# Optimization experiments

Hardware: AMD Instinct MI355X
Metric: run time of the kernel (lower is better)

Reference implementation:

```python
import jax, jax.numpy as jnp
import numpy as np


def _normalize(x, axis=-1, eps=1e-12):
    n = jnp.linalg.norm(x, axis=axis, keepdims=True)
    return x / jnp.maximum(n, eps)


def _mlp(x, w1, b1, w2, b2):
    return jnp.maximum(x @ w1 + b1, 0.0) @ w2 + b2


def _quat_mul(a, b):
    # openfold (w, x, y, z) convention, Hamilton product
    aw, ax, ay, az = a[..., 0], a[..., 1], a[..., 2], a[..., 3]
    bw, bx, by, bz = b[..., 0], b[..., 1], b[..., 2], b[..., 3]
    return jnp.stack([
        aw * bw - ax * bx - ay * by - az * bz,
        aw * bx + ax * bw + ay * bz - az * by,
        aw * by - ax * bz + ay * bw + az * bx,
        aw * bz + ax * by - ay * bx + az * bw], axis=-1)


def _quat_rotate(q, v):
    # rotate vector v by unit quaternion q
    w = q[..., :1]
    u = q[..., 1:]
    t = 2.0 * jnp.cross(u, v)
    return v + w * t + jnp.cross(u, t)


def _conj(q):
    return q * jnp.asarray([1.0, -1.0, -1.0, -1.0], dtype=q.dtype)


def setup_inputs() -> dict:
    B, N, P, H, E, M = 2, 384, 128, 64, 32, 64
    key = jax.random.key(0)
    ks = iter(jax.random.split(key, 64))

    def nrm(shape):
        return jax.random.normal(next(ks), shape, dtype=jnp.float32)

    inp = {
        "frames_q": _normalize(nrm((B, N, 4))),
        "frames_x": nrm((B, N, 3)),
        "torsions": nrm((B, N, 7, 2)),
        "h": nrm((B, N, H)),
        "e": nrm((B, N, N, E)),
        "node_mask": jnp.ones((B, N), dtype=bool),
        "pocket_h": nrm((B, P, H)),
        "pocket_e": nrm((B, N, P, E)),
        "pocket_q": _normalize(nrm((B, P, 4))),
        "pocket_x": nrm((B, P, 3)),
        "pocket_mask": jnp.ones((B, P), dtype=bool),
    }
    # 2-layer MLPs with transition_size = 64
    for name, (fin, fout) in {"msg": (2 * H + E + 9, M), "feat": (H + M, H),
                              "tr": (M, 3), "qu": (M, 4), "to": (M, 14)}.items():
        inp[f"{name}_w1"] = nrm((fin, 64)) / np.sqrt(fin)
        inp[f"{name}_b1"] = nrm((64,)) * 0.01
        inp[f"{name}_w2"] = nrm((64, fout)) / np.sqrt(64)
        inp[f"{name}_b2"] = nrm((fout,)) * 0.01
    return inp


def reference(frames_q, frames_x, torsions, h, e, node_mask, pocket_h, pocket_e,
              pocket_q, pocket_x, pocket_mask,
              msg_w1, msg_b1, msg_w2, msg_b2,
              feat_w1, feat_b1, feat_w2, feat_b2,
              tr_w1, tr_b1, tr_w2, tr_b2,
              qu_w1, qu_b1, qu_w2, qu_b2,
              to_w1, to_b1, to_w2, to_b2):
    B, N, Hd = h.shape
    P = pocket_h.shape[-2]

    q_all = jnp.concatenate([frames_q, pocket_q], axis=-2)  # [B, N+P, 4]
    x_all = jnp.concatenate([frames_x, pocket_x], axis=-2)  # [B, N+P, 3]

    eye = jnp.eye(N, dtype=bool)
    mm = jnp.concatenate([
        node_mask[:, :, None] & node_mask[:, None, :] & ~eye,
        node_mask[:, :, None] & pocket_mask[:, None, :]], axis=-1)  # [B, N, N+P]

    vec = frames_x[:, :, None, :] - x_all[:, None, :, :]  # [B, N, N+P, 3]
    d2 = jnp.sum(vec * vec, axis=-1)                       # [B, N, N+P]
    qdot = jnp.abs(jnp.sum(frames_q[:, :, None, :] * q_all[:, None, :, :], axis=-1))

    # global -> local frame of node j applied to node i: R_j^T (x_i - t_j)
    qc = _conj(q_all)[:, None, :, :]                       # [B, 1, N+P, 4]
    local_x = _quat_rotate(qc, vec)                        # [B, N, N+P, 3]
    local_q = _quat_mul(qc, jnp.broadcast_to(frames_q[:, :, None, :], (B, N, N + P, 4)))

    feat = jnp.concatenate([
        jnp.broadcast_to(h[:, :, None, :], (B, N, N + P, Hd)),
        jnp.broadcast_to(jnp.concatenate([h, pocket_h], axis=-2)[:, None, :, :], (B, N, N + P, Hd)),
        jnp.concatenate([e, pocket_e], axis=-2),
        local_x, local_q, d2[..., None], qdot[..., None]], axis=-1)

    m = _mlp(feat, msg_w1, msg_b1, msg_w2, msg_b2) * mm[..., None]  # [B, N, N+P, M]
    msum = jnp.sum(m, axis=-2)                                      # [B, N, M]

    o = _mlp(jnp.concatenate([h, msum], axis=-1), feat_w1, feat_b1, feat_w2, feat_b2)

    dx = _mlp(m, tr_w1, tr_b1, tr_w2, tr_b2) * mm[..., None]        # [B, N, N+P, 3]

    ident = jnp.asarray([1.0, 0.0, 0.0, 0.0], dtype=frames_q.dtype)
    dq = _mlp(msum, qu_w1, qu_b1, qu_w2, qu_b2)
    dq = _normalize(jnp.where(node_mask[..., None], dq, ident))
    upd_q = _quat_mul(frames_q, dq)
    upd_q = _normalize(jnp.where(node_mask[..., None], upd_q, ident))

    qn_all = _normalize(q_all)
    gdx = jnp.sum(_quat_rotate(qn_all[:, None, :, :], dx), axis=-2)  # [B, N, 3]
    n_nb = (node_mask.sum(-1) + pocket_mask.sum(-1) - 1).astype(frames_x.dtype)
    upd_x = frames_x + gdx / n_nb[:, None, None]

    upd_torsions = _normalize(_mlp(msum, to_w1, to_b1, to_w2, to_b2).reshape(torsions.shape))

    return upd_q, upd_x, upd_torsions, o
```

## Files before the change

### kernel.cpp

```cpp
#include <hip/hip_runtime.h>
#include <math.h>

#define BB 2
#define NN 384
#define PP 128
#define HH 64
#define EE 32
#define NP 512
#define K1S 136
#define K2S 72

#define X_OFF (BB*NN*4)
#define T_OFF (X_OFF + BB*NN*3)
#define O_OFF (T_OFF + BB*NN*14)

using bf16x8 = __attribute__((ext_vector_type(8))) __bf16;
using f32x4  = __attribute__((ext_vector_type(4))) float;

__device__ __forceinline__ f32x4 MFMA(bf16x8 a, bf16x8 b, f32x4 c) {
  return __builtin_amdgcn_mfma_f32_16x16x32_bf16(a, b, c, 0, 0, 0);
}
__device__ __forceinline__ bf16x8 LDF(const __bf16* base, int off) {
  return *(const bf16x8*)(base + off);
}
__device__ __forceinline__ bf16x8 pack8(f32x4 lo, f32x4 hi) {
  bf16x8 r;
  r[0]=(__bf16)lo[0]; r[1]=(__bf16)lo[1]; r[2]=(__bf16)lo[2]; r[3]=(__bf16)lo[3];
  r[4]=(__bf16)hi[0]; r[5]=(__bf16)hi[1]; r[6]=(__bf16)hi[2]; r[7]=(__bf16)hi[3];
  return r;
}
__device__ __forceinline__ bf16x8 pack8v(float4 lo, float4 hi) {
  bf16x8 r;
  r[0]=(__bf16)lo.x; r[1]=(__bf16)lo.y; r[2]=(__bf16)lo.z; r[3]=(__bf16)lo.w;
  r[4]=(__bf16)hi.x; r[5]=(__bf16)hi.y; r[6]=(__bf16)hi.z; r[7]=(__bf16)hi.w;
  return r;
}
__device__ __forceinline__ int rowpos(int n) {
  const int t = (n>>5)*2 + ((n>>2)&1);
  const int q = ((n>>3)&3)*4 + (n&3);
  return t*16 + q;
}

__global__ __launch_bounds__(512, 2) void egnn_edge_swapped(
    const float* __restrict__ frames_q, const float* __restrict__ frames_x,
    const float* __restrict__ h, const float* __restrict__ e,
    const int* __restrict__ node_mask,
    const float* __restrict__ pocket_h, const float* __restrict__ pe,
    const float* __restrict__ pocket_q, const float* __restrict__ pocket_x,
    const int* __restrict__ pocket_mask,
    const float* __restrict__ w1, const float* __restrict__ b1,
    const float* __restrict__ w2, const float* __restrict__ b2,
    const float* __restrict__ tw1, const float* __restrict__ tb1,
    const float* __restrict__ tw2, const float* __restrict__ tb2,
    float* __restrict__ msum_ws, float* __restrict__ gdx_ws)
{
  __shared__ __align__(16) __bf16 s_w1p[64*K1S];
  __shared__ __align__(16) __bf16 s_w2p[64*K2S];
  __shared__ __align__(16) __bf16 s_tw1p[64*K2S];
  __shared__ __align__(16) __bf16 s_tw2p[16*K2S];
  __shared__ __align__(16) __bf16 s_geo[NP*16 + 8];
  __shared__ __align__(16) float s_qn[NP*4];
  __shared__ float s_maskf[NP];
  __shared__ float s_b2[64], s_tb1[64], s_tb2[4];
  __shared__ float s_msum[64], s_gdx[3];

  const int tid = threadIdx.x;
  const int b = blockIdx.x / NN, i = blockIdx.x % NN;

  for (int idx = tid; idx < 64*128; idx += 512) {
    const int n = idx & 63, k = idx >> 6;
    float v = 0.f;
    if      (k < 64)  v = w1[(64 + k)*64 + n];
    else if (k < 96)  v = w1[(128 + (k-64))*64 + n];
    else if (k < 105) v = w1[(160 + (k-96))*64 + n];
    if (k != 105) s_w1p[rowpos(n)*K1S + k] = (__bf16)v;
  }
  for (int idx = tid; idx < 64*64; idx += 512) {
    const int n = idx & 63, k = idx >> 6;
    s_w2p[rowpos(n)*K2S + k]  = (__bf16)w2[k*64 + n];
    s_tw1p[rowpos(n)*K2S + k] = (__bf16)tw1[k*64 + n];
  }
  for (int idx = tid; idx < 16*64; idx += 512) {
    const int row = idx >> 6, k = idx & 63;
    s_tw2p[row*K2S + k] = (__bf16)((row < 3) ? tw2[k*3 + row] : 0.f);
  }
  if (tid < 64) { s_b2[tid] = b2[tid]; s_tb1[tid] = tb1[tid]; s_msum[tid] = 0.f; }
  if (tid < 8)  s_geo[NP*16 + tid] = (__bf16)0.f;
  if (tid < 3)  { s_tb2[tid] = tb2[tid]; s_gdx[tid] = 0.f; }

  {
    const int n = tid >> 3, part = tid & 7;
    const float* hi = &h[(b*NN + i)*HH];
    float a = 0.f;
#pragma unroll
    for (int c = 0; c < 8; ++c) a = fmaf(hi[part*8 + c], w1[(part*8 + c)*64 + n], a);
    a += __shfl_xor(a, 1); a += __shfl_xor(a, 2); a += __shfl_xor(a, 4);
    if (part == 0) s_w1p[rowpos(n)*K1S + 105] = (__bf16)(a + b1[n]);
  }

  {
    const int j = tid;
    const int maski = node_mask[b*NN + i];
    const float qi0 = frames_q[(b*NN+i)*4+0], qi1 = frames_q[(b*NN+i)*4+1],
                qi2 = frames_q[(b*NN+i)*4+2], qi3 = frames_q[(b*NN+i)*4+3];
    const float xi0 = frames_x[(b*NN+i)*3+0], xi1 = frames_x[(b*NN+i)*3+1],
                xi2 = frames_x[(b*NN+i)*3+2];
    float qj0,qj1,qj2,qj3, xj0,xj1,xj2; int mj;
    if (j < NN) {
      const float4 q4 = *(const float4*)&frames_q[(b*NN+j)*4];
      qj0=q4.x; qj1=q4.y; qj2=q4.z; qj3=q4.w;
      xj0=frames_x[(b*NN+j)*3+0]; xj1=frames_x[(b*NN+j)*3+1]; xj2=frames_x[(b*NN+j)*3+2];
      mj = (node_mask[b*NN+j] != 0) && (j != i);
    } else {
      const int jp = j - NN;
      const float4 q4 = *(const float4*)&pocket_q[(b*PP+jp)*4];
      qj0=q4.x; qj1=q4.y; qj2=q4.z; qj3=q4.w;
      xj0=pocket_x[(b*PP+jp)*3+0]; xj1=pocket_x[(b*PP+jp)*3+1]; xj2=pocket_x[(b*PP+jp)*3+2];
      mj = (pocket_mask[b*PP+jp] != 0);
    }
    const float v0 = xi0 - xj0, v1 = xi1 - xj1, v2 = xi2 - xj2;
    const float d2 = v0*v0 + v1*v1 + v2*v2;
    const float qdot = fabsf(qi0*qj0 + qi1*qj1 + qi2*qj2 + qi3*qj3);
    const float cw = qj0, cx = -qj1, cy = -qj2, cz = -qj3;
    const float t0 = 2.f*(cy*v2 - cz*v1);
    const float t1 = 2.f*(cz*v0 - cx*v2);
    const float t2 = 2.f*(cx*v1 - cy*v0);
    const float lx0 = v0 + cw*t0 + (cy*t2 - cz*t1);
    const float lx1 = v1 + cw*t1 + (cz*t0 - cx*t2);
    const float lx2 = v2 + cw*t2 + (cx*t1 - cy*t0);
    const float lq0 = cw*qi0 - cx*qi1 - cy*qi2 - cz*qi3;
    const float lq1 = cw*qi1 + cx*qi0 + cy*qi3 - cz*qi2;
    const float lq2 = cw*qi2 - cx*qi3 + cy*qi0 + cz*qi1;
    const float lq3 = cw*qi3 + cx*qi2 - cy*qi1 + cz*qi0;
    __bf16* g = &s_geo[j*16];
    g[0]=(__bf16)lx0; g[1]=(__bf16)lx1; g[2]=(__bf16)lx2; g[3]=(__bf16)lq0;
    g[4]=(__bf16)lq1; g[5]=(__bf16)lq2; g[6]=(__bf16)lq3; g[7]=(__bf16)d2;
    g[8]=(__bf16)qdot; g[9]=(__bf16)1.f;
    g[10]=(__bf16)0.f; g[11]=(__bf16)0.f; g[12]=(__bf16)0.f;
    g[13]=(__bf16)0.f; g[14]=(__bf16)0.f; g[15]=(__bf16)0.f;
    s_maskf[j] = (maski && mj) ? 1.f : 0.f;
    const float inv = 1.f / fmaxf(sqrtf(qj0*qj0 + qj1*qj1 + qj2*qj2 + qj3*qj3), 1e-12f);
    float4* qn = (float4*)&s_qn[j*4];
    *qn = make_float4(qj0*inv, qj1*inv, qj2*inv, qj3*inv);
  }
  __syncthreads();

  const int wv = tid >> 6, lane = tid & 63;
  const int l15 = lane & 15, lg = lane >> 4;

  bf16x8 tw2f[2];
  tw2f[0] = *(const bf16x8*)&s_tw2p[l15*K2S +  0 + lg*8];
  tw2f[1] = *(const bf16x8*)&s_tw2p[l15*K2S + 32 + lg*8];

  float b2r[16], tb1r[16];
#pragma unroll
  for (int t2 = 0; t2 < 4; ++t2)
#pragma unroll
    for (int r = 0; r < 4; ++r) {
      const int n2 = (t2>>1)*32 + lg*8 + (t2&1)*4 + r;
      b2r[t2*4 + r]  = s_b2[n2];
      tb1r[t2*4 + r] = s_tb1[n2];
    }
  const float tb2r0 = s_tb2[0], tb2r1 = s_tb2[1], tb2r2 = s_tb2[2];

  float msacc[16];
#pragma unroll
  for (int v = 0; v < 16; ++v) msacc[v] = 0.f;
  float gx0 = 0.f, gx1 = 0.f, gx2 = 0.f;

  const int o1base = l15*K1S + lg*8;
  const int o2base = l15*K2S + lg*8;

#define LOADSTRIP(S, H0_,H1_,H2_,H3_,E0_,E1_) do {                          \
    const int jbase_ = wv*64 + (S)*16;                                      \
    const int j_ = jbase_ + l15;                                            \
    const float *hj_, *ej_;                                                 \
    if (jbase_ < NN) {                                                      \
      hj_ = &h[(b*NN + j_)*HH];                                             \
      ej_ = &e[((b*NN + i)*NN + j_)*EE];                                    \
    } else {                                                                \
      const int jp_ = j_ - NN;                                              \
      hj_ = &pocket_h[(b*PP + jp_)*HH];                                     \
      ej_ = &pe[((b*NN + i)*PP + jp_)*EE];                                  \
    }                                                                       \
    H0_ = *(const float4*)&hj_[lg*8];                                       \
    H1_ = *(const float4*)&hj_[lg*8 + 4];                                   \
    H2_ = *(const float4*)&hj_[32 + lg*8];                                  \
    H3_ = *(const float4*)&hj_[32 + lg*8 + 4];                              \
    E0_ = *(const float4*)&ej_[lg*8];                                       \
    E1_ = *(const float4*)&ej_[lg*8 + 4];                                   \
  } while (0)

  float4 cH0, cH1, cH2, cH3, cE0, cE1;
  float4 nH0, nH1, nH2, nH3, nE0, nE1;
  LOADSTRIP(0, cH0, cH1, cH2, cH3, cE0, cE1);

#pragma unroll
  for (int s = 0; s < 4; ++s) {
    if (s < 3) LOADSTRIP(s+1, nH0, nH1, nH2, nH3, nE0, nE1);

    int o1 = o1base; asm volatile("" : "+v"(o1));
    int o2 = o2base; asm volatile("" : "+v"(o2));

    const int j = wv*64 + s*16 + l15;
    const float mask_f = s_maskf[j];

    const bf16x8 bf0 = pack8v(cH0, cH1);
    const bf16x8 bf1 = pack8v(cH2, cH3);
    const bf16x8 bf2 = pack8v(cE0, cE1);
    const bf16x8 bf3 = *(const bf16x8*)&s_geo[(lg < 2) ? (j*16 + lg*8) : NP*16];

    const f32x4 zero4 = {0.f, 0.f, 0.f, 0.f};
    f32x4 a0 = MFMA(LDF(s_w1p, o1 + 0*16*K1S +  0), bf0, zero4);
    a0 = MFMA(LDF(s_w1p, o1 + 0*16*K1S + 32), bf1, a0);
    a0 = MFMA(LDF(s_w1p, o1 + 0*16*K1S + 64), bf2, a0);
    a0 = MFMA(LDF(s_w1p, o1 + 0*16*K1S + 96), bf3, a0);
    f32x4 a1 = MFMA(LDF(s_w1p, o1 + 1*16*K1S +  0), bf0, zero4);
    a1 = MFMA(LDF(s_w1p, o1 + 1*16*K1S + 32), bf1, a1);
    a1 = MFMA(LDF(s_w1p, o1 + 1*16*K1S + 64), bf2, a1);
    a1 = MFMA(LDF(s_w1p, o1 + 1*16*K1S + 96), bf3, a1);
#pragma unroll
    for (int r = 0; r < 4; ++r) { a0[r] = fmaxf(a0[r], 0.f); a1[r] = fmaxf(a1[r], 0.f); }
    const bf16x8 hb0 = pack8(a0, a1);
    f32x4 a2 = MFMA(LDF(s_w1p, o1 + 2*16*K1S +  0), bf0, zero4);
    a2 = MFMA(LDF(s_w1p, o1 + 2*16*K1S + 32), bf1, a2);
    a2 = MFMA(LDF(s_w1p, o1 + 2*16*K1S + 64), bf2, a2);
    a2 = MFMA(LDF(s_w1p, o1 + 2*16*K1S + 96), bf3, a2);
    f32x4 a3 = MFMA(LDF(s_w1p, o1 + 3*16*K1S +  0), bf0, zero4);
    a3 = MFMA(LDF(s_w1p, o1 + 3*16*K1S + 32), bf1, a3);
    a3 = MFMA(LDF(s_w1p, o1 + 3*16*K1S + 64), bf2, a3);
    a3 = MFMA(LDF(s_w1p, o1 + 3*16*K1S + 96), bf3, a3);
#pragma unroll
    for (int r = 0; r < 4; ++r) { a2[r] = fmaxf(a2[r], 0.f); a3[r] = fmaxf(a3[r], 0.f); }
    const bf16x8 hb1 = pack8(a2, a3);

    f32x4 c0 = MFMA(LDF(s_w2p, o2 + 0*16*K2S +  0), hb0, zero4);
    c0 = MFMA(LDF(s_w2p, o2 + 0*16*K2S + 32), hb1, c0);
    f32x4 c1 = MFMA(LDF(s_w2p, o2 + 1*16*K2S +  0), hb0, zero4);
    c1 = MFMA(LDF(s_w2p, o2 + 1*16*K2S + 32), hb1, c1);
#pragma unroll
    for (int r = 0; r < 4; ++r) {
      c0[r] = (c0[r] + b2r[0*4+r]) * mask_f;  msacc[0*4+r] += c0[r];
      c1[r] = (c1[r] + b2r[1*4+r]) * mask_f;  msacc[1*4+r] += c1[r];
    }
    const bf16x8 mb0 = pack8(c0, c1);
    f32x4 c2 = MFMA(LDF(s_w2p, o2 + 2*16*K2S +  0), hb0, zero4);
    c2 = MFMA(LDF(s_w2p, o2 + 2*16*K2S + 32), hb1, c2);
    f32x4 c3 = MFMA(LDF(s_w2p, o2 + 3*16*K2S +  0), hb0, zero4);
    c3 = MFMA(LDF(s_w2p, o2 + 3*16*K2S + 32), hb1, c3);
#pragma unroll
    for (int r = 0; r < 4; ++r) {
      c2[r] = (c2[r] + b2r[2*4+r]) * mask_f;  msacc[2*4+r] += c2[r];
      c3[r] = (c3[r] + b2r[3*4+r]) * mask_f;  msacc[3*4+r] += c3[r];
    }
    const bf16x8 mb1 = pack8(c2, c3);

    f32x4 d0 = MFMA(LDF(s_tw1p, o2 + 0*16*K2S +  0), mb0, zero4);
    d0 = MFMA(LDF(s_tw1p, o2 + 0*16*K2S + 32), mb1, d0);
    f32x4 d1 = MFMA(LDF(s_tw1p, o2 + 1*16*K2S +  0), mb0, zero4);
    d1 = MFMA(LDF(s_tw1p, o2 + 1*16*K2S + 32), mb1, d1);
#pragma unroll
    for (int r = 0; r < 4; ++r) {
      d0[r] = fmaxf(d0[r] + tb1r[0*4+r], 0.f);
      d1[r] = fmaxf(d1[r] + tb1r[1*4+r], 0.f);
    }
    const bf16x8 thb0 = pack8(d0, d1);
    f32x4 d2f = MFMA(LDF(s_tw1p, o2 + 2*16*K2S +  0), mb0, zero4);
    d2f = MFMA(LDF(s_tw1p, o2 + 2*16*K2S + 32), mb1, d2f);
    f32x4 d3 = MFMA(LDF(s_tw1p, o2 + 3*16*K2S +  0), mb0, zero4);
    d3 = MFMA(LDF(s_tw1p, o2 + 3*16*K2S + 32), mb1, d3);
#pragma unroll
    for (int r = 0; r < 4; ++r) {
      d2f[r] = fmaxf(d2f[r] + tb1r[2*4+r], 0.f);
      d3[r]  = fmaxf(d3[r]  + tb1r[3*4+r], 0.f);
    }
    const bf16x8 thb1 = pack8(d2f, d3);

    f32x4 dacc = MFMA(tw2f[0], thb0, zero4);
    dacc = MFMA(tw2f[1], thb1, dacc);

    if (lg == 0) {
      const float dx0 = (dacc[0] + tb2r0) * mask_f;
      const float dx1 = (dacc[1] + tb2r1) * mask_f;
      const float dx2 = (dacc[2] + tb2r2) * mask_f;
      const float4 qn = *(const float4*)&s_qn[j*4];
      const float w = qn.x, ux = qn.y, uy = qn.z, uz = qn.w;
      const float r0 = 2.f*(uy*dx2 - uz*dx1);
      const float r1 = 2.f*(uz*dx0 - ux*dx2);
      const float r2 = 2.f*(ux*dx1 - uy*dx0);
      gx0 += dx0 + w*r0 + (uy*r2 - uz*r1);
      gx1 += dx1 + w*r1 + (uz*r0 - ux*r2);
      gx2 += dx2 + w*r2 + (ux*r1 - uy*r0);
    }

    if (s < 3) {
      cH0 = nH0; cH1 = nH1; cH2 = nH2; cH3 = nH3; cE0 = nE0; cE1 = nE1;
    }
  }
#undef LOADSTRIP

#pragma unroll
  for (int v = 0; v < 16; ++v) {
    float x = msacc[v];
    x += __shfl_xor(x, 1); x += __shfl_xor(x, 2);
    x += __shfl_xor(x, 4); x += __shfl_xor(x, 8);
    if (l15 == 0) {
      const int n2 = (v>>3)*32 + lg*8 + ((v>>2)&1)*4 + (v&3);
      atomicAdd(&s_msum[n2], x);
    }
  }
  {
    float v0 = (lg == 0) ? gx0 : 0.f;
    float v1 = (lg == 0) ? gx1 : 0.f;
    float v2 = (lg == 0) ? gx2 : 0.f;
#pragma unroll
    for (int sft = 1; sft < 64; sft <<= 1) {
      v0 += __shfl_xor(v0, sft); v1 += __shfl_xor(v1, sft); v2 += __shfl_xor(v2, sft);
    }
    if (lane == 0) { atomicAdd(&s_gdx[0], v0); atomicAdd(&s_gdx[1], v1); atomicAdd(&s_gdx[2], v2); }
  }
  __syncthreads();
  if (tid < 64) msum_ws[(b*NN + i)*64 + tid] = s_msum[tid];
  if (tid >= 64 && tid < 67) gdx_ws[(b*NN + i)*3 + (tid - 64)] = s_gdx[tid - 64];
}

__global__ __launch_bounds__(64) void egnn_node_kernel(
    const float* __restrict__ frames_q, const float* __restrict__ frames_x,
    const float* __restrict__ h,
    const int* __restrict__ node_mask, const int* __restrict__ pocket_mask,
    const float* __restrict__ fw1, const float* __restrict__ fb1,
    const float* __restrict__ fw2, const float* __restrict__ fb2,
    const float* __restrict__ qw1, const float* __restrict__ qb1,
    const float* __restrict__ qw2, const float* __restrict__ qb2,
    const float* __restrict__ tow1, const float* __restrict__ tob1,
    const float* __restrict__ tow2, const float* __restrict__ tob2,
    const float* __restrict__ msum_ws, const float* __restrict__ gdx_ws,
    float* __restrict__ out)
{
  const int t  = threadIdx.x;
  const int bi = blockIdx.x;
  const int b = bi / NN, i = bi % NN;
  __shared__ float s_h[64], s_ms[64], s_hid[64], s_tmp[16];

  s_h[t]  = h[(b*NN+i)*HH + t];
  s_ms[t] = msum_ws[(b*NN+i)*64 + t];

  int cnt = 0;
  for (int k = t; k < NN; k += 64) cnt += (node_mask[b*NN+k] != 0);
  for (int k = t; k < PP; k += 64) cnt += (pocket_mask[b*PP+k] != 0);
  cnt += __shfl_xor(cnt,1); cnt += __shfl_xor(cnt,2); cnt += __shfl_xor(cnt,4);
  cnt += __shfl_xor(cnt,8); cnt += __shfl_xor(cnt,16); cnt += __shfl_xor(cnt,32);
  const float n_nb = (float)(cnt - 1);

  __syncthreads();
  float a = fb1[t];
  for (int k = 0; k < 64; ++k) a = fmaf(s_h[k],  fw1[k*64 + t], a);
  for (int k = 0; k < 64; ++k) a = fmaf(s_ms[k], fw1[(64+k)*64 + t], a);
  s_hid[t] = fmaxf(a, 0.f);
  __syncthreads();
  float ov = fb2[t];
  for (int k = 0; k < 64; ++k) ov = fmaf(s_hid[k], fw2[k*64 + t], ov);
  out[O_OFF + (b*NN+i)*64 + t] = ov;

  __syncthreads();
  float aq = qb1[t];
  for (int k = 0; k < 64; ++k) aq = fmaf(s_ms[k], qw1[k*64 + t], aq);
  s_hid[t] = fmaxf(aq, 0.f);
  __syncthreads();
  if (t < 4) {
    float d = qb2[t];
    for (int k = 0; k < 64; ++k) d = fmaf(s_hid[k], qw2[k*4 + t], d);
    s_tmp[t] = d;
  }
  __syncthreads();
  if (t == 0) {
    const int mi = node_mask[b*NN+i];
    float d0,d1,d2,d3;
    if (mi) { d0=s_tmp[0]; d1=s_tmp[1]; d2=s_tmp[2]; d3=s_tmp[3]; }
    else    { d0=1.f; d1=0.f; d2=0.f; d3=0.f; }
    float nrm = fmaxf(sqrtf(d0*d0+d1*d1+d2*d2+d3*d3), 1e-12f);
    d0/=nrm; d1/=nrm; d2/=nrm; d3/=nrm;
    const float q0=frames_q[(b*NN+i)*4+0], q1=frames_q[(b*NN+i)*4+1],
                q2=frames_q[(b*NN+i)*4+2], q3=frames_q[(b*NN+i)*4+3];
    float u0 = q0*d0 - q1*d1 - q2*d2 - q3*d3;
    float u1 = q0*d1 + q1*d0 + q2*d3 - q3*d2;
    float u2 = q0*d2 - q1*d3 + q2*d0 + q3*d1;
    float u3 = q0*d3 + q1*d2 - q2*d1 + q3*d0;
    if (!mi) { u0=1.f; u1=0.f; u2=0.f; u3=0.f; }
    float nrm2 = fmaxf(sqrtf(u0*u0+u1*u1+u2*u2+u3*u3), 1e-12f);
    out[(b*NN+i)*4+0]=u0/nrm2; out[(b*NN+i)*4+1]=u1/nrm2;
    out[(b*NN+i)*4+2]=u2/nrm2; out[(b*NN+i)*4+3]=u3/nrm2;
  }
  if (t < 3) {
    out[X_OFF + (b*NN+i)*3 + t] = frames_x[(b*NN+i)*3+t] + gdx_ws[(b*NN+i)*3+t] / n_nb;
  }

  __syncthreads();
  float at = tob1[t];
  for (int k = 0; k < 64; ++k) at = fmaf(s_ms[k], tow1[k*64 + t], at);
  s_hid[t] = fmaxf(at, 0.f);
  __syncthreads();
  if (t < 14) {
    float v = tob2[t];
    for (int k = 0; k < 64; ++k) v = fmaf(s_hid[k], tow2[k*14 + t], v);
    s_tmp[t] = v;
  }
  __syncthreads();
  if (t < 14) {
    const int p = t & ~1;
    const float a0 = s_tmp[p], a1 = s_tmp[p+1];
    const float nrm = fmaxf(sqrtf(a0*a0 + a1*a1), 1e-12f);
    out[T_OFF + (b*NN+i)*14 + t] = s_tmp[t] / nrm;
  }
}

extern "C" void kernel_launch(void* const* d_in, const int* in_sizes, int n_in,
                              void* d_out, int out_size, void* d_ws, size_t ws_size,
                              hipStream_t stream) {
  const float* frames_q    = (const float*)d_in[0];
  const float* frames_x    = (const float*)d_in[1];
  const float* h           = (const float*)d_in[3];
  const float* e           = (const float*)d_in[4];
  const int*   node_mask   = (const int*)d_in[5];
  const float* pocket_h    = (const float*)d_in[6];
  const float* pocket_e    = (const float*)d_in[7];
  const float* pocket_q    = (const float*)d_in[8];
  const float* pocket_x    = (const float*)d_in[9];
  const int*   pocket_mask = (const int*)d_in[10];
  const float* msg_w1 = (const float*)d_in[11];
  const float* msg_b1 = (const float*)d_in[12];
  const float* msg_w2 = (const float*)d_in[13];
  const float* msg_b2 = (const float*)d_in[14];
  const float* feat_w1 = (const float*)d_in[15];
  const float* feat_b1 = (const float*)d_in[16];
  const float* feat_w2 = (const float*)d_in[17];
  const float* feat_b2 = (const float*)d_in[18];
  const float* tr_w1 = (const float*)d_in[19];
  const float* tr_b1 = (const float*)d_in[20];
  const float* tr_w2 = (const float*)d_in[21];
  const float* tr_b2 = (const float*)d_in[22];
  const float* qu_w1 = (const float*)d_in[23];
  const float* qu_b1 = (const float*)d_in[24];
  const float* qu_w2 = (const float*)d_in[25];
  const float* qu_b2 = (const float*)d_in[26];
  const float* to_w1 = (const float*)d_in[27];
  const float* to_b1 = (const float*)d_in[28];
  const float* to_w2 = (const float*)d_in[29];
  const float* to_b2 = (const float*)d_in[30];

  float* out = (float*)d_out;
  float* msum_ws = (float*)d_ws;
  float* gdx_ws  = msum_ws + BB*NN*64;

  egnn_edge_swapped<<<dim3(BB*NN), dim3(512), 0, stream>>>(
      frames_q, frames_x, h, e, node_mask,
      pocket_h, pocket_e, pocket_q, pocket_x, pocket_mask,
      msg_w1, msg_b1, msg_w2, msg_b2,
      tr_w1, tr_b1, tr_w2, tr_b2,
      msum_ws, gdx_ws);

  egnn_node_kernel<<<dim3(BB*NN), dim3(64), 0, stream>>>(
      frames_q, frames_x, h, node_mask, pocket_mask,
      feat_w1, feat_b1, feat_w2, feat_b2,
      qu_w1, qu_b1, qu_w2, qu_b2,
      to_w1, to_b1, to_w2, to_b2,
      msum_ws, gdx_ws, out);
}
```

Before: 65.92 us.

## Process two 16-neighbor strips per iteration to reuse LDS weight fragments

```diff
diff --git a/kernel.cpp b/kernel.cpp
--- a/kernel.cpp
+++ b/kernel.cpp
@@ -61,7 +61,8 @@
   __shared__ __align__(16) __bf16 s_geo[NP*16 + 8];
   __shared__ __align__(16) float s_qn[NP*4];
   __shared__ float s_maskf[NP];
-  __shared__ float s_b2[64], s_tb1[64], s_tb2[4];
+  __shared__ __align__(16) float s_b2[64], s_tb1[64];
+  __shared__ float s_tb2[4];
   __shared__ float s_msum[64], s_gdx[3];
 
   const int tid = threadIdx.x;
@@ -151,16 +152,6 @@
   bf16x8 tw2f[2];
   tw2f[0] = *(const bf16x8*)&s_tw2p[l15*K2S +  0 + lg*8];
   tw2f[1] = *(const bf16x8*)&s_tw2p[l15*K2S + 32 + lg*8];
-
-  float b2r[16], tb1r[16];
-#pragma unroll
-  for (int t2 = 0; t2 < 4; ++t2)
-#pragma unroll
-    for (int r = 0; r < 4; ++r) {
-      const int n2 = (t2>>1)*32 + lg*8 + (t2&1)*4 + r;
-      b2r[t2*4 + r]  = s_b2[n2];
-      tb1r[t2*4 + r] = s_tb1[n2];
-    }
   const float tb2r0 = s_tb2[0], tb2r1 = s_tb2[1], tb2r2 = s_tb2[2];
 
   float msacc[16];
@@ -170,12 +161,13 @@
 
   const int o1base = l15*K1S + lg*8;
   const int o2base = l15*K2S + lg*8;
-
-#define LOADSTRIP(S, H0_,H1_,H2_,H3_,E0_,E1_) do {                          \
-    const int jbase_ = wv*64 + (S)*16;                                      \
-    const int j_ = jbase_ + l15;                                            \
+  const int obbase = lg*8;
+
+#define LOADSTRIP(JB0, H0_,H1_,H2_,H3_,E0_,E1_) do {                        \
+    const int jb_ = (JB0);                                                  \
+    const int j_ = jb_ + l15;                                               \
     const float *hj_, *ej_;                                                 \
-    if (jbase_ < NN) {                                                      \
+    if (jb_ < NN) {                                                         \
       hj_ = &h[(b*NN + j_)*HH];                                             \
       ej_ = &e[((b*NN + i)*NN + j_)*EE];                                    \
     } else {                                                                \
@@ -191,110 +183,212 @@
     E1_ = *(const float4*)&ej_[lg*8 + 4];                                   \
   } while (0)
 
-  float4 cH0, cH1, cH2, cH3, cE0, cE1;
-  float4 nH0, nH1, nH2, nH3, nE0, nE1;
-  LOADSTRIP(0, cH0, cH1, cH2, cH3, cE0, cE1);
-
-#pragma unroll
-  for (int s = 0; s < 4; ++s) {
-    if (s < 3) LOADSTRIP(s+1, nH0, nH1, nH2, nH3, nE0, nE1);
-
+#pragma unroll
+  for (int ss = 0; ss < 2; ++ss) {
     int o1 = o1base; asm volatile("" : "+v"(o1));
     int o2 = o2base; asm volatile("" : "+v"(o2));
-
-    const int j = wv*64 + s*16 + l15;
-    const float mask_f = s_maskf[j];
-
-    const bf16x8 bf0 = pack8v(cH0, cH1);
-    const bf16x8 bf1 = pack8v(cH2, cH3);
-    const bf16x8 bf2 = pack8v(cE0, cE1);
-    const bf16x8 bf3 = *(const bf16x8*)&s_geo[(lg < 2) ? (j*16 + lg*8) : NP*16];
+    int ob = obbase; asm volatile("" : "+v"(ob));
+
+    const int jbA = wv*64 + ss*32;
+    const int jbB = jbA + 16;
+    const int jA = jbA + l15, jB = jbB + l15;
+
+    float4 hA0,hA1,hA2,hA3,eA0,eA1, hB0,hB1,hB2,hB3,eB0,eB1;
+    LOADSTRIP(jbA, hA0,hA1,hA2,hA3,eA0,eA1);
+    LOADSTRIP(jbB, hB0,hB1,hB2,hB3,eB0,eB1);
+    const float maskA = s_maskf[jA];
+    const float maskB = s_maskf[jB];
+
+    const bf16x8 bfA0 = pack8v(hA0, hA1);
+    const bf16x8 bfA1 = pack8v(hA2, hA3);
+    const bf16x8 bfA2 = pack8v(eA0, eA1);
+    const bf16x8 bfA3 = *(const bf16x8*)&s_geo[(lg < 2) ? (jA*16 + lg*8) : NP*16];
+    const bf16x8 bfB0 = pack8v(hB0, hB1);
+    const bf16x8 bfB1 = pack8v(hB2, hB3);
+    const bf16x8 bfB2 = pack8v(eB0, eB1);
+    const bf16x8 bfB3 = *(const bf16x8*)&s_geo[(lg < 2) ? (jB*16 + lg*8) : NP*16];
 
     const f32x4 zero4 = {0.f, 0.f, 0.f, 0.f};
-    f32x4 a0 = MFMA(LDF(s_w1p, o1 + 0*16*K1S +  0), bf0, zero4);
-    a0 = MFMA(LDF(s_w1p, o1 + 0*16*K1S + 32), bf1, a0);
-    a0 = MFMA(LDF(s_w1p, o1 + 0*16*K1S + 64), bf2, a0);
-    a0 = MFMA(LDF(s_w1p, o1 + 0*16*K1S + 96), bf3, a0);
-    f32x4 a1 = MFMA(LDF(s_w1p, o1 + 1*16*K1S +  0), bf0, zero4);
-    a1 = MFMA(LDF(s_w1p, o1 + 1*16*K1S + 32), bf1, a1);
-    a1 = MFMA(LDF(s_w1p, o1 + 1*16*K1S + 64), bf2, a1);
-    a1 = MFMA(LDF(s_w1p, o1 + 1*16*K1S + 96), bf3, a1);
-#pragma unroll
-    for (int r = 0; r < 4; ++r) { a0[r] = fmaxf(a0[r], 0.f); a1[r] = fmaxf(a1[r], 0.f); }
-    const bf16x8 hb0 = pack8(a0, a1);
-    f32x4 a2 = MFMA(LDF(s_w1p, o1 + 2*16*K1S +  0), bf0, zero4);
-    a2 = MFMA(LDF(s_w1p, o1 + 2*16*K1S + 32), bf1, a2);
-    a2 = MFMA(LDF(s_w1p, o1 + 2*16*K1S + 64), bf2, a2);
-    a2 = MFMA(LDF(s_w1p, o1 + 2*16*K1S + 96), bf3, a2);
-    f32x4 a3 = MFMA(LDF(s_w1p, o1 + 3*16*K1S +  0), bf0, zero4);
-    a3 = MFMA(LDF(s_w1p, o1 + 3*16*K1S + 32), bf1, a3);
-    a3 = MFMA(LDF(s_w1p, o1 + 3*16*K1S + 64), bf2, a3);
-    a3 = MFMA(LDF(s_w1p, o1 + 3*16*K1S + 96), bf3, a3);
-#pragma unroll
-    for (int r = 0; r < 4; ++r) { a2[r] = fmaxf(a2[r], 0.f); a3[r] = fmaxf(a3[r], 0.f); }
-    const bf16x8 hb1 = pack8(a2, a3);
-
-    f32x4 c0 = MFMA(LDF(s_w2p, o2 + 0*16*K2S +  0), hb0, zero4);
-    c0 = MFMA(LDF(s_w2p, o2 + 0*16*K2S + 32), hb1, c0);
-    f32x4 c1 = MFMA(LDF(s_w2p, o2 + 1*16*K2S +  0), hb0, zero4);
-    c1 = MFMA(LDF(s_w2p, o2 + 1*16*K2S + 32), hb1, c1);
-#pragma unroll
-    for (int r = 0; r < 4; ++r) {
-      c0[r] = (c0[r] + b2r[0*4+r]) * mask_f;  msacc[0*4+r] += c0[r];
-      c1[r] = (c1[r] + b2r[1*4+r]) * mask_f;  msacc[1*4+r] += c1[r];
-    }
-    const bf16x8 mb0 = pack8(c0, c1);
-    f32x4 c2 = MFMA(LDF(s_w2p, o2 + 2*16*K2S +  0), hb0, zero4);
-    c2 = MFMA(LDF(s_w2p, o2 + 2*16*K2S + 32), hb1, c2);
-    f32x4 c3 = MFMA(LDF(s_w2p, o2 + 3*16*K2S +  0), hb0, zero4);
-    c3 = MFMA(LDF(s_w2p, o2 + 3*16*K2S + 32), hb1, c3);
-#pragma unroll
-    for (int r = 0; r < 4; ++r) {
-      c2[r] = (c2[r] + b2r[2*4+r]) * mask_f;  msacc[2*4+r] += c2[r];
-      c3[r] = (c3[r] + b2r[3*4+r]) * mask_f;  msacc[3*4+r] += c3[r];
-    }
-    const bf16x8 mb1 = pack8(c2, c3);
-
-    f32x4 d0 = MFMA(LDF(s_tw1p, o2 + 0*16*K2S +  0), mb0, zero4);
-    d0 = MFMA(LDF(s_tw1p, o2 + 0*16*K2S + 32), mb1, d0);
-    f32x4 d1 = MFMA(LDF(s_tw1p, o2 + 1*16*K2S +  0), mb0, zero4);
-    d1 = MFMA(LDF(s_tw1p, o2 + 1*16*K2S + 32), mb1, d1);
-#pragma unroll
-    for (int r = 0; r < 4; ++r) {
-      d0[r] = fmaxf(d0[r] + tb1r[0*4+r], 0.f);
-      d1[r] = fmaxf(d1[r] + tb1r[1*4+r], 0.f);
-    }
-    const bf16x8 thb0 = pack8(d0, d1);
-    f32x4 d2f = MFMA(LDF(s_tw1p, o2 + 2*16*K2S +  0), mb0, zero4);
-    d2f = MFMA(LDF(s_tw1p, o2 + 2*16*K2S + 32), mb1, d2f);
-    f32x4 d3 = MFMA(LDF(s_tw1p, o2 + 3*16*K2S +  0), mb0, zero4);
-    d3 = MFMA(LDF(s_tw1p, o2 + 3*16*K2S + 32), mb1, d3);
-#pragma unroll
-    for (int r = 0; r < 4; ++r) {
-      d2f[r] = fmaxf(d2f[r] + tb1r[2*4+r], 0.f);
-      d3[r]  = fmaxf(d3[r]  + tb1r[3*4+r], 0.f);
-    }
-    const bf16x8 thb1 = pack8(d2f, d3);
-
-    f32x4 dacc = MFMA(tw2f[0], thb0, zero4);
-    dacc = MFMA(tw2f[1], thb1, dacc);
+
+    bf16x8 hbA0, hbA1, hbB0, hbB1;
+    {
+      f32x4 aA0, aA1, aB0, aB1;
+      {
+        const bf16x8 F0 = LDF(s_w1p, o1 + 0*16*K1S +  0);
+        const bf16x8 F1 = LDF(s_w1p, o1 + 0*16*K1S + 32);
+        const bf16x8 F2 = LDF(s_w1p, o1 + 0*16*K1S + 64);
+        const bf16x8 F3 = LDF(s_w1p, o1 + 0*16*K1S + 96);
+        aA0 = MFMA(F0,bfA0,zero4); aA0 = MFMA(F1,bfA1,aA0); aA0 = MFMA(F2,bfA2,aA0); aA0 = MFMA(F3,bfA3,aA0);
+        aB0 = MFMA(F0,bfB0,zero4); aB0 = MFMA(F1,bfB1,aB0); aB0 = MFMA(F2,bfB2,aB0); aB0 = MFMA(F3,bfB3,aB0);
+      }
+      {
+        const bf16x8 F0 = LDF(s_w1p, o1 + 1*16*K1S +  0);
+        const bf16x8 F1 = LDF(s_w1p, o1 + 1*16*K1S + 32);
+        const bf16x8 F2 = LDF(s_w1p, o1 + 1*16*K1S + 64);
+        const bf16x8 F3 = LDF(s_w1p, o1 + 1*16*K1S + 96);
+        aA1 = MFMA(F0,bfA0,zero4); aA1 = MFMA(F1,bfA1,aA1); aA1 = MFMA(F2,bfA2,aA1); aA1 = MFMA(F3,bfA3,aA1);
+        aB1 = MFMA(F0,bfB0,zero4); aB1 = MFMA(F1,bfB1,aB1); aB1 = MFMA(F2,bfB2,aB1); aB1 = MFMA(F3,bfB3,aB1);
+      }
+#pragma unroll
+      for (int r = 0; r < 4; ++r) {
+        aA0[r] = fmaxf(aA0[r], 0.f); aA1[r] = fmaxf(aA1[r], 0.f);
+        aB0[r] = fmaxf(aB0[r], 0.f); aB1[r] = fmaxf(aB1[r], 0.f);
+      }
+      hbA0 = pack8(aA0, aA1); hbB0 = pack8(aB0, aB1);
+      {
+        const bf16x8 F0 = LDF(s_w1p, o1 + 2*16*K1S +  0);
+        const bf16x8 F1 = LDF(s_w1p, o1 + 2*16*K1S + 32);
+        const bf16x8 F2 = LDF(s_w1p, o1 + 2*16*K1S + 64);
+        const bf16x8 F3 = LDF(s_w1p, o1 + 2*16*K1S + 96);
+        aA0 = MFMA(F0,bfA0,zero4); aA0 = MFMA(F1,bfA1,aA0); aA0 = MFMA(F2,bfA2,aA0); aA0 = MFMA(F3,bfA3,aA0);
+        aB0 = MFMA(F0,bfB0,zero4); aB0 = MFMA(F1,bfB1,aB0); aB0 = MFMA(F2,bfB2,aB0); aB0 = MFMA(F3,bfB3,aB0);
+      }
+      {
+        const bf16x8 F0 = LDF(s_w1p, o1 + 3*16*K1S +  0);
+        const bf16x8 F1 = LDF(s_w1p, o1 + 3*16*K1S + 32);
+        const bf16x8 F2 = LDF(s_w1p, o1 + 3*16*K1S + 64);
+        const bf16x8 F3 = LDF(s_w1p, o1 + 3*16*K1S + 96);
+        aA1 = MFMA(F0,bfA0,zero4); aA1 = MFMA(F1,bfA1,aA1); aA1 = MFMA(F2,bfA2,aA1); aA1 = MFMA(F3,bfA3,aA1);
+        aB1 = MFMA(F0,bfB0,zero4); aB1 = MFMA(F1,bfB1,aB1); aB1 = MFMA(F2,bfB2,aB1); aB1 = MFMA(F3,bfB3,aB1);
+      }
+#pragma unroll
+      for (int r = 0; r < 4; ++r) {
+        aA0[r] = fmaxf(aA0[r], 0.f); aA1[r] = fmaxf(aA1[r], 0.f);
+        aB0[r] = fmaxf(aB0[r], 0.f); aB1[r] = fmaxf(aB1[r], 0.f);
+      }
+      hbA1 = pack8(aA0, aA1); hbB1 = pack8(aB0, aB1);
+    }
+
+    bf16x8 mbA0, mbA1, mbB0, mbB1;
+    {
+      f32x4 cA0, cA1, cB0, cB1;
+      {
+        const bf16x8 F0 = LDF(s_w2p, o2 + 0*16*K2S +  0);
+        const bf16x8 F1 = LDF(s_w2p, o2 + 0*16*K2S + 32);
+        cA0 = MFMA(F0,hbA0,zero4); cA0 = MFMA(F1,hbA1,cA0);
+        cB0 = MFMA(F0,hbB0,zero4); cB0 = MFMA(F1,hbB1,cB0);
+      }
+      {
+        const bf16x8 F0 = LDF(s_w2p, o2 + 1*16*K2S +  0);
+        const bf16x8 F1 = LDF(s_w2p, o2 + 1*16*K2S + 32);
+        cA1 = MFMA(F0,hbA0,zero4); cA1 = MFMA(F1,hbA1,cA1);
+        cB1 = MFMA(F0,hbB0,zero4); cB1 = MFMA(F1,hbB1,cB1);
+      }
+      const f32x4 bb0 = *(const f32x4*)&s_b2[ob + 0];
+      const f32x4 bb1 = *(const f32x4*)&s_b2[ob + 4];
+#pragma unroll
+      for (int r = 0; r < 4; ++r) {
+        cA0[r] = (cA0[r] + bb0[r]) * maskA;  cB0[r] = (cB0[r] + bb0[r]) * maskB;
+        cA1[r] = (cA1[r] + bb1[r]) * maskA;  cB1[r] = (cB1[r] + bb1[r]) * maskB;
+        msacc[0*4+r] += cA0[r] + cB0[r];
+        msacc[1*4+r] += cA1[r] + cB1[r];
+      }
+      mbA0 = pack8(cA0, cA1); mbB0 = pack8(cB0, cB1);
+      {
+        const bf16x8 F0 = LDF(s_w2p, o2 + 2*16*K2S +  0);
+        const bf16x8 F1 = LDF(s_w2p, o2 + 2*16*K2S + 32);
+        cA0 = MFMA(F0,hbA0,zero4); cA0 = MFMA(F1,hbA1,cA0);
+        cB0 = MFMA(F0,hbB0,zero4); cB0 = MFMA(F1,hbB1,cB0);
+      }
+      {
+        const bf16x8 F0 = LDF(s_w2p, o2 + 3*16*K2S +  0);
+        const bf16x8 F1 = LDF(s_w2p, o2 + 3*16*K2S + 32);
+        cA1 = MFMA(F0,hbA0,zero4); cA1 = MFMA(F1,hbA1,cA1);
+        cB1 = MFMA(F0,hbB0,zero4); cB1 = MFMA(F1,hbB1,cB1);
+      }
+      const f32x4 bb2 = *(const f32x4*)&s_b2[ob + 32];
+      const f32x4 bb3 = *(const f32x4*)&s_b2[ob + 36];
+#pragma unroll
+      for (int r = 0; r < 4; ++r) {
+        cA0[r] = (cA0[r] + bb2[r]) * maskA;  cB0[r] = (cB0[r] + bb2[r]) * maskB;
+        cA1[r] = (cA1[r] + bb3[r]) * maskA;  cB1[r] = (cB1[r] + bb3[r]) * maskB;
+        msacc[2*4+r] += cA0[r] + cB0[r];
+        msacc[3*4+r] += cA1[r] + cB1[r];
+      }
+      mbA1 = pack8(cA0, cA1); mbB1 = pack8(cB0, cB1);
+    }
+
+    bf16x8 thbA0, thbA1, thbB0, thbB1;
+    {
+      f32x4 dA0, dA1, dB0, dB1;
+      {
+        const bf16x8 F0 = LDF(s_tw1p, o2 + 0*16*K2S +  0);
+        const bf16x8 F1 = LDF(s_tw1p, o2 + 0*16*K2S + 32);
+        dA0 = MFMA(F0,mbA0,zero4); dA0 = MFMA(F1,mbA1,dA0);
+        dB0 = MFMA(F0,mbB0,zero4); dB0 = MFMA(F1,mbB1,dB0);
+      }
+      {
+        const bf16x8 F0 = LDF(s_tw1p, o2 + 1*16*K2S +  0);
+        const bf16x8 F1 = LDF(s_tw1p, o2 + 1*16*K2S + 32);
+        dA1 = MFMA(F0,mbA0,zero4); dA1 = MFMA(F1,mbA1,dA1);
+        dB1 = MFMA(F0,mbB0,zero4); dB1 = MFMA(F1,mbB1,dB1);
+      }
+      {
+        const f32x4 tb0 = *(const f32x4*)&s_tb1[ob + 0];
+        const f32x4 tb1v = *(const f32x4*)&s_tb1[ob + 4];
+#pragma unroll
+        for (int r = 0; r < 4; ++r) {
+          dA0[r] = fmaxf(dA0[r] + tb0[r], 0.f);  dB0[r] = fmaxf(dB0[r] + tb0[r], 0.f);
+          dA1[r] = fmaxf(dA1[r] + tb1v[r], 0.f); dB1[r] = fmaxf(dB1[r] + tb1v[r], 0.f);
+        }
+      }
+      thbA0 = pack8(dA0, dA1); thbB0 = pack8(dB0, dB1);
+      {
+        const bf16x8 F0 = LDF(s_tw1p, o2 + 2*16*K2S +  0);
+        const bf16x8 F1 = LDF(s_tw1p, o2 + 2*16*K2S + 32);
+        dA0 = MFMA(F0,mbA0,zero4); dA0 = MFMA(F1,mbA1,dA0);
+        dB0 = MFMA(F0,mbB0,zero4); dB0 = MFMA(F1,mbB1,dB0);
+      }
+      {
+        const bf16x8 F0 = LDF(s_tw1p, o2 + 3*16*K2S +  0);
+        const bf16x8 F1 = LDF(s_tw1p, o2 + 3*16*K2S + 32);
+        dA1 = MFMA(F0,mbA0,zero4); dA1 = MFMA(F1,mbA1,dA1);
+        dB1 = MFMA(F0,mbB0,zero4); dB1 = MFMA(F1,mbB1,dB1);
+      }
+      {
+        const f32x4 tb2v = *(const f32x4*)&s_tb1[ob + 32];
+        const f32x4 tb3v = *(const f32x4*)&s_tb1[ob + 36];
+#pragma unroll
+        for (int r = 0; r < 4; ++r) {
+          dA0[r] = fmaxf(dA0[r] + tb2v[r], 0.f);  dB0[r] = fmaxf(dB0[r] + tb2v[r], 0.f);
+          dA1[r] = fmaxf(dA1[r] + tb3v[r], 0.f);  dB1[r] = fmaxf(dB1[r] + tb3v[r], 0.f);
+        }
+      }
+      thbA1 = pack8(dA0, dA1); thbB1 = pack8(dB0, dB1);
+    }
+
+    f32x4 daccA = MFMA(tw2f[0], thbA0, zero4);
+    daccA = MFMA(tw2f[1], thbA1, daccA);
+    f32x4 daccB = MFMA(tw2f[0], thbB0, zero4);
+    daccB = MFMA(tw2f[1], thbB1, daccB);
 
     if (lg == 0) {
-      const float dx0 = (dacc[0] + tb2r0) * mask_f;
-      const float dx1 = (dacc[1] + tb2r1) * mask_f;
-      const float dx2 = (dacc[2] + tb2r2) * mask_f;
-      const float4 qn = *(const float4*)&s_qn[j*4];
-      const float w = qn.x, ux = qn.y, uy = qn.z, uz = qn.w;
-      const float r0 = 2.f*(uy*dx2 - uz*dx1);
-      const float r1 = 2.f*(uz*dx0 - ux*dx2);
-      const float r2 = 2.f*(ux*dx1 - uy*dx0);
-      gx0 += dx0 + w*r0 + (uy*r2 - uz*r1);
-      gx1 += dx1 + w*r1 + (uz*r0 - ux*r2);
-      gx2 += dx2 + w*r2 + (ux*r1 - uy*r0);
-    }
-
-    if (s < 3) {
-      cH0 = nH0; cH1 = nH1; cH2 = nH2; cH3 = nH3; cE0 = nE0; cE1 = nE1;
+      {
+        const float dx0 = (daccA[0] + tb2r0) * maskA;
+        const float dx1 = (daccA[1] + tb2r1) * maskA;
+        const float dx2 = (daccA[2] + tb2r2) * maskA;
+        const float4 qn = *(const float4*)&s_qn[jA*4];
+        const float w = qn.x, ux = qn.y, uy = qn.z, uz = qn.w;
+        const float r0 = 2.f*(uy*dx2 - uz*dx1);
+        const float r1 = 2.f*(uz*dx0 - ux*dx2);
+        const float r2 = 2.f*(ux*dx1 - uy*dx0);
+        gx0 += dx0 + w*r0 + (uy*r2 - uz*r1);
+        gx1 += dx1 + w*r1 + (uz*r0 - ux*r2);
+        gx2 += dx2 + w*r2 + (ux*r1 - uy*r0);
+      }
+      {
+        const float dx0 = (daccB[0] + tb2r0) * maskB;
+        const float dx1 = (daccB[1] + tb2r1) * maskB;
+        const float dx2 = (daccB[2] + tb2r2) * maskB;
+        const float4 qn = *(const float4*)&s_qn[jB*4];
+        const float w = qn.x, ux = qn.y, uy = qn.z, uz = qn.w;
+        const float r0 = 2.f*(uy*dx2 - uz*dx1);
+        const float r1 = 2.f*(uz*dx0 - ux*dx2);
+        const float r2 = 2.f*(ux*dx1 - uy*dx0);
+        gx0 += dx0 + w*r0 + (uy*r2 - uz*r1);
+        gx1 += dx1 + w*r1 + (uz*r0 - ux*r2);
+        gx2 += dx2 + w*r2 + (ux*r1 - uy*r0);
+      }
     }
   }
 #undef LOADSTRIP
```

After: 65.02 us. No clear change (-1.4%).
